# Performance work log

Hardware: AMD Instinct MI355X
Metric: run time of the kernel (lower is better)

Reference implementation:

```python
import jax, jax.numpy as jnp
import numpy as np

B, S, D = 1, 2048, 4096
H, KVH, HD = 32, 8, 128
ROPE_THETA = 10000.0
RMS_EPS = 1e-5


def setup_inputs() -> dict:
    key = jax.random.key(0)
    k1, k2, k3 = jax.random.split(key, 3)
    scale = 1.0 / np.sqrt(D)
    return {
        "inputs_embeds": jax.random.normal(k1, (B, S, D), dtype=jnp.float32),
        "attention_mask": jnp.ones((B, S), dtype=jnp.float32),
        "g": jnp.ones((D,), dtype=jnp.float32),
        "Wq": jax.random.normal(k2, (D, H * HD), dtype=jnp.float32) * scale,
        "Wk": jax.random.normal(k3, (D, KVH * HD), dtype=jnp.float32) * scale,
    }


def _rotate_half(x):
    return jnp.concatenate([-x[..., HD // 2:], x[..., :HD // 2]], axis=-1)


def reference(inputs_embeds, attention_mask, g, Wq, Wk):
    # RMSNorm
    var = jnp.mean(jnp.square(inputs_embeds), axis=-1, keepdims=True)
    h = inputs_embeds * jax.lax.rsqrt(var + RMS_EPS) * g

    # QK projections -> [B, heads, S, HD]
    q = (h @ Wq).reshape(B, S, H, HD).transpose(0, 2, 1, 3)
    k = (h @ Wk).reshape(B, S, KVH, HD).transpose(0, 2, 1, 3)

    # RoPE (llama-style: cos/sin of duplicated half-dim freqs)
    pos = jnp.arange(S, dtype=jnp.float32)
    inv_freq = 1.0 / (ROPE_THETA ** (jnp.arange(0, HD, 2, dtype=jnp.float32) / HD))
    freqs = pos[:, None] * inv_freq[None, :]            # [S, HD/2]
    emb = jnp.concatenate([freqs, freqs], axis=-1)       # [S, HD]
    cos = jnp.cos(emb)[None, None]                       # [1,1,S,HD]
    sin = jnp.sin(emb)[None, None]
    q = q * cos + _rotate_half(q) * sin
    k = k * cos + _rotate_half(k) * sin

    # repeat_kv: expand KV heads to H query heads (grouped-query)
    k = jnp.repeat(k, H // KVH, axis=1)                  # [B,H,S,HD]

    # raw QK^T scores (no softmax/V)
    scores = jnp.einsum('bhqd,bhkd->bhqk', q, k) / np.float32(np.sqrt(HD))

    # causal mask + 2D padding mask (all-ones here -> pure causal)
    min_f = jnp.finfo(scores.dtype).min
    i = jnp.arange(S)[:, None]
    j = jnp.arange(S)[None, :]
    causal = jnp.where(j > i, min_f, jnp.float32(0.0))   # [S,S]
    pad = (causal[None, None] == 0.0) & (attention_mask[:, None, None, :] == 0.0)
    mask = jnp.where(pad, min_f, causal[None, None])     # [B,1,S,S]
    return scores + mask
```

## Files before the change

### kernel.cpp

```cpp
#include <hip/hip_runtime.h>
#include <hip/hip_bf16.h>
#include <math.h>

#define S_LEN 2048
#define D_DIM 4096
#define NTOT 5120

typedef _Float16 f16x8 __attribute__((ext_vector_type(8)));
typedef float f32x4 __attribute__((ext_vector_type(4)));

#define MASKF (-3.3895313892515355e+38f)

#define QCH_BASE 134217728ull
#define KCH_BASE 201326592ull

__device__ __forceinline__ void async_ld16(const void* g, void* l) {
  __builtin_amdgcn_global_load_lds((const __attribute__((address_space(1))) void*)g,
                                   (__attribute__((address_space(3))) void*)l, 16, 0, 0);
}

__global__ __launch_bounds__(256) void prep(const float* __restrict__ x,
                                            const float* __restrict__ g,
                                            _Float16* __restrict__ h,
                                            float* __restrict__ ct, float* __restrict__ st) {
  int b = blockIdx.x;
  if (b >= 2048) {
    int i = (b - 2048) * 256 + threadIdx.x;
    int s = i >> 6, f = i & 63;
    float inv = (float)(1.0 / pow(10000.0, (double)(2 * f) / 128.0));
    float ang = (float)s * inv;
    ct[i] = (float)cos((double)ang);
    st[i] = (float)sin((double)ang);
    return;
  }
  int s = b;
  int t = threadIdx.x, w = t >> 6, l = t & 63;
  const f32x4* xr = (const f32x4*)(x + (size_t)s * D_DIM);
  const f32x4* gr = (const f32x4*)g;
  f32x4 v[4];
  float ss = 0.f;
#pragma unroll
  for (int i = 0; i < 4; ++i) {
    v[i] = xr[t + i * 256];
    ss += v[i][0] * v[i][0] + v[i][1] * v[i][1] + v[i][2] * v[i][2] + v[i][3] * v[i][3];
  }
#pragma unroll
  for (int off = 32; off; off >>= 1) ss += __shfl_down(ss, off);
  __shared__ float red[4];
  if (l == 0) red[w] = ss;
  __syncthreads();
  float tot = red[0] + red[1] + red[2] + red[3];
  float scale = rsqrtf(tot * (1.f / D_DIM) + 1e-5f);
  _Float16* hr = h + (size_t)s * D_DIM;
#pragma unroll
  for (int i = 0; i < 4; ++i) {
    f32x4 gg = gr[t + i * 256];
    _Float16 o[4];
    o[0] = (_Float16)(v[i][0] * scale * gg[0]);
    o[1] = (_Float16)(v[i][1] * scale * gg[1]);
    o[2] = (_Float16)(v[i][2] * scale * gg[2]);
    o[3] = (_Float16)(v[i][3] * scale * gg[3]);
    *(short4*)(hr + (size_t)(t + i * 256) * 4) = *(short4*)o;
  }
}

__global__ __launch_bounds__(256) void transpose_both(const float* __restrict__ Wq,
                                                      const float* __restrict__ Wk,
                                                      _Float16* __restrict__ wt) {
  __shared__ float tile[32][33];
  int b = blockIdx.x;
  const float* W;
  _Float16* Wt;
  int N, tn, td;
  if (b < 16384) {
    W = Wq; Wt = wt; N = 4096;
    tn = b & 127; td = b >> 7;
  } else {
    int b2 = b - 16384;
    W = Wk; Wt = wt + (size_t)4096 * D_DIM; N = 1024;
    tn = b2 & 31; td = b2 >> 5;
  }
  int c = threadIdx.x & 31, r0 = threadIdx.x >> 5;
  int d0 = td * 32, n0 = tn * 32;
#pragma unroll
  for (int i = 0; i < 4; ++i) {
    int r = r0 + i * 8;
    tile[r][c] = W[(size_t)(d0 + r) * N + n0 + c];
  }
  __syncthreads();
#pragma unroll
  for (int i = 0; i < 4; ++i) {
    int r = r0 + i * 8;
    Wt[(size_t)(n0 + r) * D_DIM + d0 + c] = (_Float16)tile[c][r];
  }
}

__global__ __launch_bounds__(256, 2) void gemm_rope(const _Float16* __restrict__ A,
                                                    const _Float16* __restrict__ Bt,
                                                    const float* __restrict__ ct,
                                                    const float* __restrict__ st,
                                                    char* __restrict__ base, int K) {
  __shared__ _Float16 lds[128 * 128];
  _Float16* As = lds;
  _Float16* Bs = lds + 128 * 64;
  const int bid = blockIdx.x;
  const int xcd = bid & 7, idx = bid >> 3;
  const int flat = xcd * 80 + idx;
  const int bx = flat >> 4;
  const int by = flat & 15;
  const int brow = by * 128;
  const size_t bcol = (size_t)bx * 128;
  const int tid = threadIdx.x, w = tid >> 6, l = tid & 63;
  const int wr = w * 32;
  f32x4 acc[2][8] = {};

  int st_o[4], st_r[4], st_src[4];
#pragma unroll
  for (int p = 0; p < 4; ++p) {
    int ob = (p * 4 + w) * 1024;
    int o = ob + l * 16;
    int r = o >> 7;
    int slot = (o >> 4) & 7;
    st_o[p] = ob; st_r[p] = r; st_src[p] = slot ^ (r & 7);
  }

  for (int k0 = 0; k0 < K; k0 += 64) {
#pragma unroll
    for (int p = 0; p < 4; ++p) {
      async_ld16(A + (size_t)(brow + st_r[p]) * K + (k0 + st_src[p] * 8), (char*)As + st_o[p]);
      async_ld16(Bt + (bcol + st_r[p]) * K + (k0 + st_src[p] * 8), (char*)Bs + st_o[p]);
    }
    asm volatile("s_waitcnt vmcnt(0)" ::: "memory");
    __syncthreads();
#pragma unroll
    for (int ks = 0; ks < 2; ++ks) {
      int kslot = ks * 4 + (l >> 4);
      f16x8 af[2], bf[8];
#pragma unroll
      for (int m = 0; m < 2; ++m) {
        int row = wr + m * 16 + (l & 15);
        af[m] = *(const f16x8*)((const char*)As + row * 128 + ((kslot ^ (row & 7)) << 4));
      }
#pragma unroll
      for (int n = 0; n < 8; ++n) {
        int row = n * 16 + (l & 15);
        bf[n] = *(const f16x8*)((const char*)Bs + row * 128 + ((kslot ^ (row & 7)) << 4));
      }
#pragma unroll
      for (int m = 0; m < 2; ++m)
#pragma unroll
        for (int n = 0; n < 8; ++n)
          acc[m][n] = __builtin_amdgcn_mfma_f32_16x16x32_f16(af[m], bf[n], acc[m][n], 0, 0, 0);
    }
    __syncthreads();
  }

#pragma unroll
  for (int m = 0; m < 2; ++m)
#pragma unroll
    for (int n = 0; n < 8; ++n) {
      int col = n * 16 + (l & 15);
      int f = col & 63;
#pragma unroll
      for (int j = 0; j < 4; ++j) {
        int row = wr + m * 16 + ((l >> 4) << 2) + j;
        int s = brow + row;
        float v = acc[m][n][j];
        float p = acc[m][n ^ 4][j];
        float o = v * ct[s * 64 + f] + ((col < 64) ? -p : p) * st[s * 64 + f];
        lds[row * 128 + (col ^ ((row & 7) << 3))] = (_Float16)o;
      }
    }
  __syncthreads();

  {
    int row = tid >> 1, hh = tid & 1;
    int s = brow + row;
    int sw = (row & 7) << 3;
    int h = bx;
    char* dst;
    if (h < 32) {
      int cc = 2 * s + (h >> 4);
      dst = base + QCH_BASE + (size_t)(cc >> 10) * 16777216ull +
            (size_t)(cc & 1023) * 8192ull + 4096ull + (size_t)((h & 15) * 128 + hh * 64) * 2;
    } else {
      int kv = h - 32;
      dst = base + KCH_BASE + (size_t)(s >> 1) * 8192ull + 4096ull +
            (size_t)(s & 1) * 2048ull + (size_t)(kv * 128 + hh * 64) * 2;
    }
#pragma unroll
    for (int k = 0; k < 8; ++k) {
      int c = hh * 64 + k * 8;
      f16x8 vv = *(const f16x8*)&lds[row * 128 + (c ^ sw)];
      *(f16x8*)(dst + k * 16) = vv;
    }
  }
}

__device__ __forceinline__ void fill_tile_f32(float* __restrict__ outh, int qi, int kj) {
  f32x4 mv = {MASKF, MASKF, MASKF, MASKF};
  int rr = threadIdx.x >> 5, cc = threadIdx.x & 31;
#pragma unroll
  for (int i = 0; i < 16; ++i) {
    int r = qi * 128 + i * 8 + rr;
    ((f32x4*)(outh + (size_t)r * S_LEN + kj * 128))[cc] = mv;
  }
}

__global__ __launch_bounds__(256, 2) void qk_full(const char* __restrict__ base,
                                                  const float* __restrict__ am,
                                                  float* __restrict__ out) {
  __shared__ _Float16 Qs[128 * 128], Ks[128 * 128];
  const int h = blockIdx.y;
  const int qi = blockIdx.x >> 4, kj = blockIdx.x & 15;
  if (h >= 8 && h <= 12 && qi < 8 && kj >= 8) return;
  float* outh = out + (size_t)h * S_LEN * S_LEN;
  if (kj > qi) { fill_tile_f32(outh, qi, kj); return; }

  const int tid = threadIdx.x, w = tid >> 6, l = tid & 63;
  const int wr = (w >> 1) * 64, wc = (w & 1) * 64;
  const int hb = h >> 4;
  const size_t hoff = (size_t)(h & 15) * 256;
  const size_t kvoff = (size_t)(h >> 2) * 256;
#pragma unroll
  for (int p = 0; p < 8; ++p) {
    int ob = (p * 4 + w) * 1024;
    int o = ob + l * 16;
    int r = o >> 8;
    int slot = (o >> 4) & 15;
    int src = slot ^ (r & 7);
    int s = qi * 128 + r;
    int cc = 2 * s + hb;
    const char* qa = base + QCH_BASE + (size_t)(cc >> 10) * 16777216ull +
                     (size_t)(cc & 1023) * 8192ull + 4096ull + hoff + src * 16;
    int s2 = kj * 128 + r;
    const char* ka = base + KCH_BASE + (size_t)(s2 >> 1) * 8192ull + 4096ull +
                     (size_t)(s2 & 1) * 2048ull + kvoff + src * 16;
    async_ld16(qa, (char*)Qs + ob);
    async_ld16(ka, (char*)Ks + ob);
  }
  asm volatile("s_waitcnt vmcnt(0)" ::: "memory");
  __syncthreads();

  f32x4 acc[4][4] = {};
#pragma unroll
  for (int ks = 0; ks < 4; ++ks) {
    int kslot = ks * 4 + (l >> 4);
    f16x8 af[4], bf[4];
#pragma unroll
    for (int m = 0; m < 4; ++m) {
      int row = wr + m * 16 + (l & 15);
      af[m] = *(const f16x8*)((const char*)Qs + row * 256 + ((kslot ^ (row & 7)) << 4));
    }
#pragma unroll
    for (int n = 0; n < 4; ++n) {
      int row = wc + n * 16 + (l & 15);
      bf[n] = *(const f16x8*)((const char*)Ks + row * 256 + ((kslot ^ (row & 7)) << 4));
    }
#pragma unroll
    for (int m = 0; m < 4; ++m)
#pragma unroll
      for (int n = 0; n < 4; ++n)
        acc[m][n] = __builtin_amdgcn_mfma_f32_16x16x32_f16(af[m], bf[n], acc[m][n], 0, 0, 0);
  }

  const float sc = 0.088388347648318447f;
#pragma unroll
  for (int m = 0; m < 4; ++m) {
    int ib = qi * 128 + wr + m * 16 + ((l >> 4) << 2);
#pragma unroll
    for (int n = 0; n < 4; ++n) {
      int jg = kj * 128 + wc + n * 16 + (l & 15);
      float amv = am[jg];
#pragma unroll
      for (int j = 0; j < 4; ++j) {
        int i = ib + j;
        float v = acc[m][n][j] * sc;
        v = (v != v) ? 0.f : fminf(fmaxf(v, -3.38e38f), 3.38e38f);
        if (jg > i || amv == 0.f) v = MASKF;
        outh[(size_t)i * S_LEN + jg] = v;
      }
    }
  }
}

__global__ void fill_last(float* __restrict__ out) {
  int b = blockIdx.x;
  int h = 8 + (b >> 6);
  int t = b & 63;
  int qi = t >> 3, kj = 8 + (t & 7);
  fill_tile_f32(out + (size_t)h * S_LEN * S_LEN, qi, kj);
}

extern "C" void kernel_launch(void* const* d_in, const int* in_sizes, int n_in,
                              void* d_out, int out_size, void* d_ws, size_t ws_size,
                              hipStream_t stream) {
  const float* x  = (const float*)d_in[0];
  const float* am = (const float*)d_in[1];
  const float* g  = (const float*)d_in[2];
  const float* Wq = (const float*)d_in[3];
  const float* Wk = (const float*)d_in[4];
  float* out = (float*)d_out;
  char* ob = (char*)d_out;
  (void)d_ws; (void)ws_size;

  float*    ct   = (float*)(ob);
  float*    st   = (float*)(ob + 524288ull);
  _Float16* h16  = (_Float16*)(ob + 1048576ull);
  _Float16* wt   = (_Float16*)(ob + 17825792ull);

  prep<<<dim3(2560), dim3(256), 0, stream>>>(x, g, h16, ct, st);
  transpose_both<<<dim3(20480), dim3(256), 0, stream>>>(Wq, Wk, wt);
  gemm_rope<<<dim3(640), dim3(256), 0, stream>>>(h16, wt, ct, st, ob, 4096);
  qk_full<<<dim3(256, 32), dim3(256), 0, stream>>>(ob, am, out);
  fill_last<<<dim3(320), dim3(256), 0, stream>>>(out);
}
```

Measured before the change: 285.6 us.

## Use 2x2 wave tiling in QK projection GEMM and move RoPE into fp32 LDS epilogue

The projection GEMM's wave layout changes from four 32x128 row strips to a 2x2 grid of 64x64 tiles. This cuts the LDS fragment reads per MFMA, since each wave loads 4 A and 4 B fragments instead of 2 A and 8 B. Because a wave no longer holds both RoPE halves of a head, the accumulators are staged as fp32 in a 64KB LDS buffer. The rotation is then applied during the coalesced write-out, with cos/sin read per row. The larger shared memory footprint may limit the two-blocks-per-CU occupancy, and the epilogue now does more LDS traffic.

```diff
diff --git a/kernel.cpp b/kernel.cpp
--- a/kernel.cpp
+++ b/kernel.cpp
@@ -100,9 +100,10 @@
                                                     const float* __restrict__ ct,
                                                     const float* __restrict__ st,
                                                     char* __restrict__ base, int K) {
-  __shared__ _Float16 lds[128 * 128];
-  _Float16* As = lds;
-  _Float16* Bs = lds + 128 * 64;
+  __shared__ char smem[65536];
+  _Float16* As = (_Float16*)smem;
+  _Float16* Bs = (_Float16*)(smem + 16384);
+  float* fbuf = (float*)smem;
   const int bid = blockIdx.x;
   const int xcd = bid & 7, idx = bid >> 3;
   const int flat = xcd * 80 + idx;
@@ -111,8 +112,8 @@
   const int brow = by * 128;
   const size_t bcol = (size_t)bx * 128;
   const int tid = threadIdx.x, w = tid >> 6, l = tid & 63;
-  const int wr = w * 32;
-  f32x4 acc[2][8] = {};
+  const int wr = (w >> 1) * 64, wc = (w & 1) * 64;
+  f32x4 acc[4][4] = {};
 
   int st_o[4], st_r[4], st_src[4];
 #pragma unroll
@@ -135,48 +136,44 @@
 #pragma unroll
     for (int ks = 0; ks < 2; ++ks) {
       int kslot = ks * 4 + (l >> 4);
-      f16x8 af[2], bf[8];
-#pragma unroll
-      for (int m = 0; m < 2; ++m) {
+      f16x8 af[4], bf[4];
+#pragma unroll
+      for (int m = 0; m < 4; ++m) {
         int row = wr + m * 16 + (l & 15);
         af[m] = *(const f16x8*)((const char*)As + row * 128 + ((kslot ^ (row & 7)) << 4));
       }
 #pragma unroll
-      for (int n = 0; n < 8; ++n) {
-        int row = n * 16 + (l & 15);
+      for (int n = 0; n < 4; ++n) {
+        int row = wc + n * 16 + (l & 15);
         bf[n] = *(const f16x8*)((const char*)Bs + row * 128 + ((kslot ^ (row & 7)) << 4));
       }
 #pragma unroll
-      for (int m = 0; m < 2; ++m)
-#pragma unroll
-        for (int n = 0; n < 8; ++n)
+      for (int m = 0; m < 4; ++m)
+#pragma unroll
+        for (int n = 0; n < 4; ++n)
           acc[m][n] = __builtin_amdgcn_mfma_f32_16x16x32_f16(af[m], bf[n], acc[m][n], 0, 0, 0);
     }
     __syncthreads();
   }
 
 #pragma unroll
-  for (int m = 0; m < 2; ++m)
-#pragma unroll
-    for (int n = 0; n < 8; ++n) {
-      int col = n * 16 + (l & 15);
-      int f = col & 63;
+  for (int m = 0; m < 4; ++m)
+#pragma unroll
+    for (int n = 0; n < 4; ++n)
 #pragma unroll
       for (int j = 0; j < 4; ++j) {
         int row = wr + m * 16 + ((l >> 4) << 2) + j;
-        int s = brow + row;
-        float v = acc[m][n][j];
-        float p = acc[m][n ^ 4][j];
-        float o = v * ct[s * 64 + f] + ((col < 64) ? -p : p) * st[s * 64 + f];
-        lds[row * 128 + (col ^ ((row & 7) << 3))] = (_Float16)o;
-      }
-    }
+        int col = wc + n * 16 + (l & 15);
+        fbuf[row * 128 + (col ^ ((row & 7) << 3))] = acc[m][n][j];
+      }
   __syncthreads();
 
   {
     int row = tid >> 1, hh = tid & 1;
     int s = brow + row;
     int sw = (row & 7) << 3;
+    const float* ctr = ct + s * 64;
+    const float* str = st + s * 64;
     int h = bx;
     char* dst;
     if (h < 32) {
@@ -191,8 +188,18 @@
 #pragma unroll
     for (int k = 0; k < 8; ++k) {
       int c = hh * 64 + k * 8;
-      f16x8 vv = *(const f16x8*)&lds[row * 128 + (c ^ sw)];
-      *(f16x8*)(dst + k * 16) = vv;
+      f32x4 va = *(f32x4*)&fbuf[row * 128 + (c ^ sw)];
+      f32x4 vb = *(f32x4*)&fbuf[row * 128 + ((c + 4) ^ sw)];
+      f32x4 pa = *(f32x4*)&fbuf[row * 128 + ((c ^ 64) ^ sw)];
+      f32x4 pb = *(f32x4*)&fbuf[row * 128 + (((c + 4) ^ 64) ^ sw)];
+      f16x8 o;
+#pragma unroll
+      for (int u = 0; u < 4; ++u) {
+        int f = k * 8 + u;
+        o[u]     = (_Float16)(va[u] * ctr[f]     + (hh ? pa[u] : -pa[u]) * str[f]);
+        o[4 + u] = (_Float16)(vb[u] * ctr[f + 4] + (hh ? pb[u] : -pb[u]) * str[f + 4]);
+      }
+      *(f16x8*)(dst + k * 16) = o;
     }
   }
 }
```

Result: slower. 316.6 us (+10.9%).
